# Optimization experiments

Measured on AMD Instinct MI355X. Metric: run time of the kernel, lower is better.

The kernel has to match this reference:

```python
import jax, jax.numpy as jnp
import numpy as np

EPS = 1e-8

def setup_inputs() -> dict:
    key = jax.random.key(0)
    ks = jax.random.split(key, 8)
    B, D, N, F = 8192, 1024, 2048, 8
    d2 = D // 2
    # integer-valued data (IDF acts on integers)
    x = jnp.round(jax.random.normal(ks[0], (B, D), jnp.float32) * 5.0)
    s1 = 1.0 / np.sqrt(d2)
    s2 = 1.0 / np.sqrt(N)
    return {
        "x": x,
        "W1": jax.random.normal(ks[1], (F, d2, N), jnp.float32) * s1,
        "b1": jax.random.normal(ks[2], (F, N), jnp.float32) * 0.01,
        "W2": jax.random.normal(ks[3], (F, N, N), jnp.float32) * s2,
        "b2": jax.random.normal(ks[4], (F, N), jnp.float32) * 0.01,
        "W3": jax.random.normal(ks[5], (F, N, d2), jnp.float32) * s2,
        "b3": jax.random.normal(ks[6], (F, d2), jnp.float32) * 0.01,
        "mean": jnp.zeros((1, D), jnp.float32),
        "log_scale": jnp.ones((1, D), jnp.float32),
    }

def _st_round(v):
    # straight-through round: forward round, identity gradient
    return v + jax.lax.stop_gradient(jnp.round(v) - v)

def _flow(x, W1, b1, W2, b2, W3, b3):
    d2 = x.shape[1] // 2
    def step(z, p):
        w1, bb1, w2, bb2, w3, bb3 = p
        xa, xb = z[:, :d2], z[:, d2:]
        h = jax.nn.leaky_relu(xa @ w1 + bb1)          # [B, N]
        h = jax.nn.leaky_relu(h @ w2 + bb2)           # [B, N]
        t = h @ w3 + bb3                               # [B, d2]
        yb = xb + _st_round(t)
        z = jnp.concatenate([xa, yb], axis=1)[:, ::-1]  # coupling + flip permute
        return z, None
    z, _ = jax.lax.scan(step, x, (W1, b1, W2, b2, W3, b3))
    return z

def reference(x, W1, b1, W2, b2, W3, b3, mean, log_scale):
    z = _flow(x, W1, b1, W2, b2, W3, b3)
    # discretized logistic log-prior: log(sig((z+.5-m)/s) - sig((z-.5-m)/s))
    scale = jnp.exp(log_scale)
    la = jax.nn.log_sigmoid((z + 0.5 - mean) / scale)
    lb = jax.nn.log_sigmoid((z - 0.5 - mean) / scale)
    log_p = la + jnp.log(1.0 - jnp.exp(lb - la) + EPS)  # log_min_exp
    return -log_p.sum(axis=1).mean()  # reduction='avg'
```

## Files before the change

### kernel.cpp

```cpp
#include <hip/hip_runtime.h>
#include <hip/hip_bf16.h>
#include <cmath>


typedef __bf16 bf16_t;
typedef bf16_t bf16x8 __attribute__((ext_vector_type(8)));
typedef float floatx4 __attribute__((ext_vector_type(4)));

#define BQ 8192
#define DD 1024
#define D2 512
#define NH 2048
#define NF 8

__device__ __forceinline__ void gload_lds16(const void* g, void* l) {
    __builtin_amdgcn_global_load_lds(
        (__attribute__((address_space(1))) void*)g,
        (__attribute__((address_space(3))) void*)l, 16, 0, 0);
}

__global__ __launch_bounds__(256)
void transpose_bf16(const float* __restrict__ W, bf16_t* __restrict__ Wt,
                    int K, int N) {
    __shared__ float tile[32][33];
    size_t fo = (size_t)blockIdx.z * K * N;
    int n0 = blockIdx.x * 32, k0 = blockIdx.y * 32;
    int tx = threadIdx.x & 31, ty = threadIdx.x >> 5;
    for (int i = 0; i < 4; i++)
        tile[ty + i*8][tx] = W[fo + (size_t)(k0 + ty + i*8) * N + n0 + tx];
    __syncthreads();
    for (int i = 0; i < 4; i++)
        Wt[fo + (size_t)(n0 + ty + i*8) * K + k0 + tx] = (bf16_t)tile[tx][ty + i*8];
}

__global__ __launch_bounds__(256)
void copy_x(const float4* __restrict__ x, float4* __restrict__ S) {
    int idx = blockIdx.x * blockDim.x + threadIdx.x;
    S[idx] = x[idx];
}

__global__ __launch_bounds__(256)
void prep_A(const float* __restrict__ S, bf16_t* __restrict__ Ab) {
    int idx = blockIdx.x * blockDim.x + threadIdx.x;
    int m = idx >> 9;
    int j = idx & 511;
    Ab[idx] = (bf16_t)S[(size_t)m * DD + j];
}

template<int MODE, int K, int TM, int TN, int MINW>
__global__ __launch_bounds__(256, MINW)
void gemm_kernel(const bf16_t* __restrict__ A, const bf16_t* __restrict__ Bt,
                 const float* __restrict__ bias,
                 bf16_t* __restrict__ Cout, float* __restrict__ S,
                 bf16_t* __restrict__ Abn,
                 int N, int rflag)
{
    constexpr int IM   = TM / 32;
    constexpr int JN   = TN / 32;
    constexpr int NA   = TM / 64;
    constexpr int NBD  = TN / 64;
    constexpr int NDMA = NA + NBD;
    constexpr int T    = K / 32;
    static_assert((T - 1) % 3 == 0, "pipeline triple-unroll needs (T-1)%3==0");
    static_assert(JN % 4 == 0, "bff processed in groups of 4");

    __shared__ __align__(16) bf16_t As[3][TM * 32];
    __shared__ __align__(16) bf16_t Bs[3][TN * 32];

    const int tid  = threadIdx.x;
    const int lane = tid & 63;
    const int wave = tid >> 6;
    const int wm   = wave >> 1;
    const int wn   = wave & 1;
    const int m0   = blockIdx.y * TM;
    const int n0   = blockIdx.x * TN;

    const int srow = tid >> 2;
    const int sq   = ((tid & 3) ^ ((srow >> 1) & 3)) * 8;
    const bf16_t* agp = A  + (size_t)(m0 + srow) * K + sq;
    const bf16_t* bgp = Bt + (size_t)(n0 + srow) * K + sq;

    floatx4 acc[IM][JN];
#pragma unroll
    for (int i = 0; i < IM; i++)
#pragma unroll
        for (int j = 0; j < JN; j++)
            acc[i][j] = (floatx4){0.f, 0.f, 0.f, 0.f};

    const int fr  = lane & 15;
    const int fp8 = ((lane >> 4) ^ ((lane >> 1) & 3)) * 8;

#define ISSUE_TILE(NB)                                                       \
    {                                                                        \
        _Pragma("unroll")                                                    \
        for (int u = 0; u < NA; u++)                                         \
            gload_lds16(agp + (size_t)(u*64) * K, &As[NB][u*2048 + tid*8]);  \
        _Pragma("unroll")                                                    \
        for (int u = 0; u < NBD; u++)                                        \
            gload_lds16(bgp + (size_t)(u*64) * K, &Bs[NB][u*2048 + tid*8]);  \
        agp += 32; bgp += 32;                                                \
    }

#define COMPUTE(CB)                                                          \
    {                                                                        \
        bf16x8 af[IM];                                                       \
        _Pragma("unroll")                                                    \
        for (int i = 0; i < IM; i++)                                         \
            af[i] = *(const bf16x8*)&As[CB][(wm*(TM/2) + i*16 + fr)*32 + fp8];\
        _Pragma("unroll")                                                    \
        for (int g2 = 0; g2 < JN/4; g2++) {                                  \
            bf16x8 bff[4];                                                   \
            _Pragma("unroll")                                                \
            for (int j = 0; j < 4; j++)                                      \
                bff[j] = *(const bf16x8*)                                    \
                    &Bs[CB][(wn*(TN/2) + (g2*4+j)*16 + fr)*32 + fp8];        \
            _Pragma("unroll")                                                \
            for (int i = 0; i < IM; i++)                                     \
                _Pragma("unroll")                                            \
                for (int j = 0; j < 4; j++)                                  \
                    acc[i][g2*4+j] = __builtin_amdgcn_mfma_f32_16x16x32_bf16(\
                                    af[i], bff[j], acc[i][g2*4+j], 0, 0, 0); \
        }                                                                    \
    }

#define PIPE_STEP(NB, CB)                                                    \
    {                                                                        \
        ISSUE_TILE(NB);                                                      \
        __builtin_amdgcn_s_waitcnt(0x0F70 | NDMA);     \
        __builtin_amdgcn_s_barrier();                                        \
        COMPUTE(CB);                                                         \
    }

    ISSUE_TILE(0);

#pragma unroll 1
    for (int g = 0; g < (T - 1) / 3; ++g) {
        PIPE_STEP(1, 0);
        PIPE_STEP(2, 1);
        PIPE_STEP(0, 2);
    }
    __builtin_amdgcn_s_waitcnt(0x0F70);
    __builtin_amdgcn_s_barrier();
    COMPUTE(0);

#undef PIPE_STEP
#undef COMPUTE
#undef ISSUE_TILE

    const int ccol  = lane & 15;
    const int crow4 = (lane >> 4) * 4;
#pragma unroll
    for (int j = 0; j < JN; j++) {
        int col = n0 + wn*(TN/2) + j*16 + ccol;
        float bj = bias[col];
        if (MODE == 0) {
#pragma unroll
            for (int i = 0; i < IM; i++) {
#pragma unroll
                for (int r = 0; r < 4; r++) {
                    int row = m0 + wm*(TM/2) + i*16 + crow4 + r;
                    float v = acc[i][j][r] + bj;
                    v = v >= 0.f ? v : 0.01f * v;
                    Cout[(size_t)row * N + col] = (bf16_t)v;
                }
            }
        } else {
            int slot = rflag ? (511 - col) : (512 + col);
            int aj   = 511 - col;
#pragma unroll
            for (int i = 0; i < IM; i++) {
#pragma unroll
                for (int r = 0; r < 4; r++) {
                    int row = m0 + wm*(TM/2) + i*16 + crow4 + r;
                    float t = acc[i][j][r] + bj;
                    float nv = S[(size_t)row * DD + slot] + rintf(t);
                    S[(size_t)row * DD + slot] = nv;
                    Abn[(size_t)row * D2 + aj] = (bf16_t)nv;
                }
            }
        }
    }
}

__global__ __launch_bounds__(256)
void reduce_nll(const float* __restrict__ S, const float* __restrict__ mean,
                const float* __restrict__ log_scale, float* __restrict__ out)
{
    float local = 0.f;
    const int total = BQ * DD;
    for (int idx = blockIdx.x * blockDim.x + threadIdx.x; idx < total;
         idx += gridDim.x * blockDim.x) {
        int j = idx & (DD - 1);
        float z  = S[idx];
        float mu = mean[j];
        float sc = expf(log_scale[j]);
        float ua = (z + 0.5f - mu) / sc;
        float ub = (z - 0.5f - mu) / sc;
        float la = fminf(ua, 0.f) - log1pf(expf(-fabsf(ua)));
        float lb = fminf(ub, 0.f) - log1pf(expf(-fabsf(ub)));
        float lp = la + logf(1.0f - expf(lb - la) + 1e-8f);
        local += lp;
    }
    __shared__ float red[256];
    red[threadIdx.x] = local;
    __syncthreads();
    for (int s = 128; s > 0; s >>= 1) {
        if (threadIdx.x < s) red[threadIdx.x] += red[threadIdx.x + s];
        __syncthreads();
    }
    if (threadIdx.x == 0) atomicAdd(out, -red[0] * (1.0f / (float)BQ));
}

extern "C" void kernel_launch(void* const* d_in, const int* in_sizes, int n_in,
                              void* d_out, int out_size, void* d_ws, size_t ws_size,
                              hipStream_t stream)
{
    const float* x   = (const float*)d_in[0];
    const float* W1  = (const float*)d_in[1];
    const float* b1  = (const float*)d_in[2];
    const float* W2  = (const float*)d_in[3];
    const float* b2  = (const float*)d_in[4];
    const float* W3  = (const float*)d_in[5];
    const float* b3  = (const float*)d_in[6];
    const float* mean = (const float*)d_in[7];
    const float* lsc  = (const float*)d_in[8];

    char* ws = (char*)d_ws;
    bf16_t* Wt1 = (bf16_t*)ws; ws += (size_t)NF * NH * D2 * 2;
    bf16_t* Wt2 = (bf16_t*)ws; ws += (size_t)NF * NH * NH * 2;
    bf16_t* Wt3 = (bf16_t*)ws; ws += (size_t)NF * D2 * NH * 2;
    float*  S   = (float*)ws;  ws += (size_t)BQ * DD * 4;
    bf16_t* Ab  = (bf16_t*)ws; ws += (size_t)BQ * D2 * 2;
    bf16_t* H1  = (bf16_t*)ws; ws += (size_t)BQ * NH * 2;
    bf16_t* H2  = (bf16_t*)ws;

    hipMemsetAsync(d_out, 0, sizeof(float), stream);

    dim3 blk(256);
    transpose_bf16<<<dim3(NH/32, D2/32, NF), blk, 0, stream>>>(W1, Wt1, D2, NH);
    transpose_bf16<<<dim3(NH/32, NH/32, NF), blk, 0, stream>>>(W2, Wt2, NH, NH);
    transpose_bf16<<<dim3(D2/32, NH/32, NF), blk, 0, stream>>>(W3, Wt3, NH, D2);

    copy_x<<<BQ * DD / 4 / 256, blk, 0, stream>>>((const float4*)x, (float4*)S);
    prep_A<<<BQ * D2 / 256, blk, 0, stream>>>(S, Ab);

    for (int f = 0; f < NF; ++f) {
        int r = f & 1;
        gemm_kernel<0, D2, 128, 256, 2><<<dim3(NH/256, BQ/128), blk, 0, stream>>>(
            Ab, Wt1 + (size_t)f * NH * D2, b1 + (size_t)f * NH, H1, nullptr,
            nullptr, NH, 0);
        gemm_kernel<0, NH, 128, 256, 2><<<dim3(NH/256, BQ/128), blk, 0, stream>>>(
            H1, Wt2 + (size_t)f * NH * NH, b2 + (size_t)f * NH, H2, nullptr,
            nullptr, NH, 0);
        gemm_kernel<1, NH, 64, 128, 3><<<dim3(D2/128, BQ/64), blk, 0, stream>>>(
            H2, Wt3 + (size_t)f * D2 * NH, b3 + (size_t)f * D2, nullptr, S,
            Ab, D2, r);
    }

    reduce_nll<<<2048, blk, 0, stream>>>(S, mean, lsc, (float*)d_out);
}
```

Measured before the change: 1.481 ms.

## Add 256x256-tile 8-wave pipelined GEMM for the two hidden-layer matmuls

Adds a new GEMM kernel with 256x256 output tiles, 512 threads (8 waves), double-buffered LDS fed by direct global-to-LDS loads, and a fine-grained interleaving of LDS reads, next-tile loads and MFMA quarters guarded by barriers and priority hints. It replaces the 128x256 kernel for the first two layers of each flow step. The goal is more data reuse per byte loaded and better overlap of memory traffic with matrix-core work on the dominant N×N GEMM. The cost is a larger LDS footprint (128KB per block) and more registers, which limits occupancy, plus waitcnt constants hand-tuned to the exact load counts.

```diff
diff --git a/kernel.cpp b/kernel.cpp
--- a/kernel.cpp
+++ b/kernel.cpp
@@ -182,6 +182,175 @@
     }
 }
 
+template<int K>
+__global__ __launch_bounds__(512, 2)
+void gemm256_kernel(const bf16_t* __restrict__ A, const bf16_t* __restrict__ Bt,
+                    const float* __restrict__ bias, bf16_t* __restrict__ Cout,
+                    int N)
+{
+    constexpr int T = K / 64;
+    static_assert(T >= 4, "pipeline needs >=4 K-tiles");
+
+    __shared__ __align__(16) bf16_t As[2][16384];
+    __shared__ __align__(16) bf16_t Bs[2][16384];
+
+    const int tid  = threadIdx.x;
+    const int lane = tid & 63;
+    const int wave = tid >> 6;
+    const int wm   = wave >> 2;
+    const int wn   = wave & 3;
+    const int m0   = blockIdx.y * 256;
+    const int n0   = blockIdx.x * 256;
+
+    const int srow = tid >> 3;
+    const int sq   = ((tid & 7) ^ (srow & 7)) * 8;
+    const bf16_t* agp = A  + (size_t)(m0 + srow) * K + sq;
+    const bf16_t* bgp = Bt + (size_t)(n0 + srow) * K + sq;
+    const int ldst = tid * 8;
+
+#define STAGE_A(H, TILE, BUF)                                                 \
+    {                                                                         \
+        _Pragma("unroll")                                                     \
+        for (int u = 0; u < 2; ++u)                                           \
+            gload_lds16(agp + (size_t)((H)*128 + u*64) * K + (size_t)(TILE)*64,\
+                        &As[BUF][(H)*8192 + u*4096 + ldst]);                  \
+    }
+#define STAGE_B(H, TILE, BUF)                                                 \
+    {                                                                         \
+        _Pragma("unroll")                                                     \
+        for (int u = 0; u < 2; ++u)                                           \
+            gload_lds16(bgp + (size_t)((H)*128 + u*64) * K + (size_t)(TILE)*64,\
+                        &Bs[BUF][(H)*8192 + u*4096 + ldst]);                  \
+    }
+#define MFMA16(D, Av, Bv) \
+    D = __builtin_amdgcn_mfma_f32_16x16x32_bf16(Av, Bv, D, 0, 0, 0)
+
+    floatx4 acc[8][4];
+#pragma unroll
+    for (int i = 0; i < 8; ++i)
+#pragma unroll
+        for (int j = 0; j < 4; ++j)
+            acc[i][j] = (floatx4){0.f, 0.f, 0.f, 0.f};
+
+    const int fr = lane & 15;
+    const int l7 = lane & 7;
+    const int qh = lane >> 4;
+    const int ra = (wm*128 + fr) * 64;
+    const int rb = (wn*64  + fr) * 64;
+    const int c0 = ((qh    ) ^ l7) * 8;
+    const int c1 = ((qh + 4) ^ l7) * 8;
+
+    STAGE_B(0, 0, 0); STAGE_B(1, 0, 0);
+    STAGE_A(0, 0, 0); STAGE_A(1, 0, 0);
+    STAGE_B(0, 1, 1); STAGE_B(1, 1, 1);
+    __builtin_amdgcn_s_waitcnt(0x0F74);
+    __builtin_amdgcn_s_barrier();
+
+#pragma unroll 1
+    for (int tau = 0; tau < T; ++tau) {
+        const int c = tau & 1;
+        const bf16_t* Ac = As[c];
+        const bf16_t* Bc = Bs[c];
+        bf16x8 af[4][2], b01[2][2], b23[2][2];
+
+#pragma unroll
+        for (int i = 0; i < 4; ++i) {
+            af[i][0] = *(const bf16x8*)&Ac[ra + i*1024 + c0];
+            af[i][1] = *(const bf16x8*)&Ac[ra + i*1024 + c1];
+        }
+#pragma unroll
+        for (int j = 0; j < 2; ++j) {
+            b01[j][0] = *(const bf16x8*)&Bc[rb + j*1024 + c0];
+            b01[j][1] = *(const bf16x8*)&Bc[rb + j*1024 + c1];
+        }
+        if (tau + 1 < T) STAGE_A(0, tau + 1, c ^ 1);
+        __builtin_amdgcn_s_barrier();
+        __builtin_amdgcn_s_setprio(1);
+#pragma unroll
+        for (int i = 0; i < 4; ++i)
+#pragma unroll
+            for (int j = 0; j < 2; ++j) {
+                MFMA16(acc[i][j], af[i][0], b01[j][0]);
+                MFMA16(acc[i][j], af[i][1], b01[j][1]);
+            }
+        __builtin_amdgcn_s_setprio(0);
+        __builtin_amdgcn_s_barrier();
+
+#pragma unroll
+        for (int j = 0; j < 2; ++j) {
+            b23[j][0] = *(const bf16x8*)&Bc[rb + (j+2)*1024 + c0];
+            b23[j][1] = *(const bf16x8*)&Bc[rb + (j+2)*1024 + c1];
+        }
+        if (tau + 1 < T) STAGE_A(1, tau + 1, c ^ 1);
+        __builtin_amdgcn_s_barrier();
+        __builtin_amdgcn_s_setprio(1);
+#pragma unroll
+        for (int i = 0; i < 4; ++i)
+#pragma unroll
+            for (int j = 0; j < 2; ++j) {
+                MFMA16(acc[i][j+2], af[i][0], b23[j][0]);
+                MFMA16(acc[i][j+2], af[i][1], b23[j][1]);
+            }
+        __builtin_amdgcn_s_setprio(0);
+        __builtin_amdgcn_s_barrier();
+
+#pragma unroll
+        for (int i = 0; i < 4; ++i) {
+            af[i][0] = *(const bf16x8*)&Ac[ra + (i+4)*1024 + c0];
+            af[i][1] = *(const bf16x8*)&Ac[ra + (i+4)*1024 + c1];
+        }
+        if (tau + 2 < T) STAGE_B(0, tau + 2, c);
+        __builtin_amdgcn_s_barrier();
+        __builtin_amdgcn_s_setprio(1);
+#pragma unroll
+        for (int i = 0; i < 4; ++i)
+#pragma unroll
+            for (int j = 0; j < 2; ++j) {
+                MFMA16(acc[i+4][j+2], af[i][0], b23[j][0]);
+                MFMA16(acc[i+4][j+2], af[i][1], b23[j][1]);
+            }
+        __builtin_amdgcn_s_setprio(0);
+        __builtin_amdgcn_s_barrier();
+
+        if (tau + 2 < T) STAGE_B(1, tau + 2, c);
+        __builtin_amdgcn_s_barrier();
+        __builtin_amdgcn_s_setprio(1);
+#pragma unroll
+        for (int i = 0; i < 4; ++i)
+#pragma unroll
+            for (int j = 0; j < 2; ++j) {
+                MFMA16(acc[i+4][j], af[i][0], b01[j][0]);
+                MFMA16(acc[i+4][j], af[i][1], b01[j][1]);
+            }
+        __builtin_amdgcn_s_setprio(0);
+        if (tau < T - 2)       __builtin_amdgcn_s_waitcnt(0x0F74);
+        else if (tau == T - 2) __builtin_amdgcn_s_waitcnt(0x0F70);
+        __builtin_amdgcn_s_barrier();
+    }
+
+#undef STAGE_A
+#undef STAGE_B
+#undef MFMA16
+
+    const int ccol  = lane & 15;
+    const int crow4 = (lane >> 4) * 4;
+#pragma unroll
+    for (int j = 0; j < 4; ++j) {
+        int col = n0 + wn*64 + j*16 + ccol;
+        float bj = bias[col];
+#pragma unroll
+        for (int i = 0; i < 8; ++i) {
+#pragma unroll
+            for (int r = 0; r < 4; ++r) {
+                int row = m0 + wm*128 + i*16 + crow4 + r;
+                float v = acc[i][j][r] + bj;
+                v = v >= 0.f ? v : 0.01f * v;
+                Cout[(size_t)row * N + col] = (bf16_t)v;
+            }
+        }
+    }
+}
+
 __global__ __launch_bounds__(256)
 void reduce_nll(const float* __restrict__ S, const float* __restrict__ mean,
                 const float* __restrict__ log_scale, float* __restrict__ out)
@@ -246,12 +415,10 @@
 
     for (int f = 0; f < NF; ++f) {
         int r = f & 1;
-        gemm_kernel<0, D2, 128, 256, 2><<<dim3(NH/256, BQ/128), blk, 0, stream>>>(
-            Ab, Wt1 + (size_t)f * NH * D2, b1 + (size_t)f * NH, H1, nullptr,
-            nullptr, NH, 0);
-        gemm_kernel<0, NH, 128, 256, 2><<<dim3(NH/256, BQ/128), blk, 0, stream>>>(
-            H1, Wt2 + (size_t)f * NH * NH, b2 + (size_t)f * NH, H2, nullptr,
-            nullptr, NH, 0);
+        gemm256_kernel<D2><<<dim3(NH/256, BQ/256), dim3(512), 0, stream>>>(
+            Ab, Wt1 + (size_t)f * NH * D2, b1 + (size_t)f * NH, H1, NH);
+        gemm256_kernel<NH><<<dim3(NH/256, BQ/256), dim3(512), 0, stream>>>(
+            H1, Wt2 + (size_t)f * NH * NH, b2 + (size_t)f * NH, H2, NH);
         gemm_kernel<1, NH, 64, 128, 3><<<dim3(D2/128, BQ/64), blk, 0, stream>>>(
             H2, Wt3 + (size_t)f * D2 * NH, b3 + (size_t)f * D2, nullptr, S,
             Ab, D2, r);
```

Result: slower. 1.602 ms (+8.2%).

## Add double-buffered 128x128 GEMM for hidden layers and fuse input prep kernels

Applied to the files above, without the earlier changes.

Adds a new GEMM kernel with a simple two-stage LDS double buffer (async global-to-LDS loads of the next K tile overlapped with MFMA compute on the current one). The first two hidden-layer GEMMs use it with 128x128 tiles in place of the 128x256 triple-stage pipelined kernel, which doubles the grid size. The copy_x and prep_A kernels are also merged into one init kernel that writes both the float state and the bf16 half. Smaller tiles raise occupancy and parallelism but reduce reuse of each loaded tile, and the shallower pipeline may hide less memory latency.

```diff
diff --git a/kernel.cpp b/kernel.cpp
--- a/kernel.cpp
+++ b/kernel.cpp
@@ -4,6 +4,7 @@
 
 
 typedef __bf16 bf16_t;
+typedef bf16_t bf16x4 __attribute__((ext_vector_type(4)));
 typedef bf16_t bf16x8 __attribute__((ext_vector_type(8)));
 typedef float floatx4 __attribute__((ext_vector_type(4)));
 
@@ -34,17 +35,19 @@
 }
 
 __global__ __launch_bounds__(256)
-void copy_x(const float4* __restrict__ x, float4* __restrict__ S) {
+void init_SA(const float4* __restrict__ x, float4* __restrict__ S,
+             bf16_t* __restrict__ Ab) {
     int idx = blockIdx.x * blockDim.x + threadIdx.x;
-    S[idx] = x[idx];
-}
-
-__global__ __launch_bounds__(256)
-void prep_A(const float* __restrict__ S, bf16_t* __restrict__ Ab) {
-    int idx = blockIdx.x * blockDim.x + threadIdx.x;
-    int m = idx >> 9;
-    int j = idx & 511;
-    Ab[idx] = (bf16_t)S[(size_t)m * DD + j];
+    float4 v = x[idx];
+    S[idx] = v;
+    int col4 = idx & (DD/4 - 1);
+    if (col4 < D2/4) {
+        int m = idx >> 8;
+        bf16x4 p;
+        p[0] = (bf16_t)v.x; p[1] = (bf16_t)v.y;
+        p[2] = (bf16_t)v.z; p[3] = (bf16_t)v.w;
+        ((bf16x4*)Ab)[(size_t)m * (D2/4) + col4] = p;
+    }
 }
 
 template<int MODE, int K, int TM, int TN, int MINW>
@@ -177,6 +180,115 @@
                     S[(size_t)row * DD + slot] = nv;
                     Abn[(size_t)row * D2 + aj] = (bf16_t)nv;
                 }
+            }
+        }
+    }
+}
+
+template<int K, int TM, int TN>
+__global__ __launch_bounds__(256, 2)
+void gemm2b_kernel(const bf16_t* __restrict__ A, const bf16_t* __restrict__ Bt,
+                   const float* __restrict__ bias, bf16_t* __restrict__ Cout,
+                   int N)
+{
+    constexpr int IM   = TM / 32;
+    constexpr int JN   = TN / 32;
+    constexpr int NA   = TM / 64;
+    constexpr int NBD  = TN / 64;
+    constexpr int T    = K / 32;
+    static_assert(T >= 2, "need >=2 K-tiles");
+    static_assert(JN % 4 == 0, "bff processed in groups of 4");
+
+    __shared__ __align__(16) bf16_t As[2][TM * 32];
+    __shared__ __align__(16) bf16_t Bs[2][TN * 32];
+
+    const int tid  = threadIdx.x;
+    const int lane = tid & 63;
+    const int wave = tid >> 6;
+    const int wm   = wave >> 1;
+    const int wn   = wave & 1;
+    const int m0   = blockIdx.y * TM;
+    const int n0   = blockIdx.x * TN;
+
+    const int srow = tid >> 2;
+    const int sq   = ((tid & 3) ^ ((srow >> 1) & 3)) * 8;
+    const bf16_t* agp = A  + (size_t)(m0 + srow) * K + sq;
+    const bf16_t* bgp = Bt + (size_t)(n0 + srow) * K + sq;
+
+    floatx4 acc[IM][JN];
+#pragma unroll
+    for (int i = 0; i < IM; i++)
+#pragma unroll
+        for (int j = 0; j < JN; j++)
+            acc[i][j] = (floatx4){0.f, 0.f, 0.f, 0.f};
+
+    const int fr  = lane & 15;
+    const int fp8 = ((lane >> 4) ^ ((lane >> 1) & 3)) * 8;
+
+#define ISSUE_TILE(NB)                                                       \
+    {                                                                        \
+        _Pragma("unroll")                                                    \
+        for (int u = 0; u < NA; u++)                                         \
+            gload_lds16(agp + (size_t)(u*64) * K, &As[NB][u*2048 + tid*8]);  \
+        _Pragma("unroll")                                                    \
+        for (int u = 0; u < NBD; u++)                                        \
+            gload_lds16(bgp + (size_t)(u*64) * K, &Bs[NB][u*2048 + tid*8]);  \
+        agp += 32; bgp += 32;                                                \
+    }
+
+#define COMPUTE(CB)                                                          \
+    {                                                                        \
+        bf16x8 af[IM];                                                       \
+        _Pragma("unroll")                                                    \
+        for (int i = 0; i < IM; i++)                                         \
+            af[i] = *(const bf16x8*)&As[CB][(wm*(TM/2) + i*16 + fr)*32 + fp8];\
+        _Pragma("unroll")                                                    \
+        for (int g2 = 0; g2 < JN/4; g2++) {                                  \
+            bf16x8 bff[4];                                                   \
+            _Pragma("unroll")                                                \
+            for (int j = 0; j < 4; j++)                                      \
+                bff[j] = *(const bf16x8*)                                    \
+                    &Bs[CB][(wn*(TN/2) + (g2*4+j)*16 + fr)*32 + fp8];        \
+            _Pragma("unroll")                                                \
+            for (int i = 0; i < IM; i++)                                     \
+                _Pragma("unroll")                                            \
+                for (int j = 0; j < 4; j++)                                  \
+                    acc[i][g2*4+j] = __builtin_amdgcn_mfma_f32_16x16x32_bf16(\
+                                    af[i], bff[j], acc[i][g2*4+j], 0, 0, 0); \
+        }                                                                    \
+    }
+
+    ISSUE_TILE(0);
+    __builtin_amdgcn_s_waitcnt(0x0F70);
+    __builtin_amdgcn_s_barrier();
+
+#pragma unroll 1
+    for (int tau = 0; tau < T; ++tau) {
+        if (tau + 1 < T) ISSUE_TILE((tau + 1) & 1);
+        COMPUTE(tau & 1);
+        if (tau + 1 < T) {
+            __builtin_amdgcn_s_waitcnt(0x0F70);
+            __builtin_amdgcn_s_barrier();
+        }
+    }
+
+#undef COMPUTE
+#undef ISSUE_TILE
+
+    const int ccol  = lane & 15;
+    const int crow4 = (lane >> 4) * 4;
+#pragma unroll
+    for (int j = 0; j < JN; j++) {
+        int col = n0 + wn*(TN/2) + j*16 + ccol;
+        float bj = bias[col];
+#pragma unroll
+        for (int i = 0; i < IM; i++) {
+#pragma unroll
+            for (int r = 0; r < 4; r++) {
+                int row = m0 + wm*(TM/2) + i*16 + crow4 + r;
+                float v = acc[i][j][r] + bj;
+                v = v >= 0.f ? v : 0.01f * v;
+                Cout[(size_t)row * N + col] = (bf16_t)v;
             }
         }
     }
@@ -241,17 +353,14 @@
     transpose_bf16<<<dim3(NH/32, NH/32, NF), blk, 0, stream>>>(W2, Wt2, NH, NH);
     transpose_bf16<<<dim3(D2/32, NH/32, NF), blk, 0, stream>>>(W3, Wt3, NH, D2);
 
-    copy_x<<<BQ * DD / 4 / 256, blk, 0, stream>>>((const float4*)x, (float4*)S);
-    prep_A<<<BQ * D2 / 256, blk, 0, stream>>>(S, Ab);
+    init_SA<<<BQ * DD / 4 / 256, blk, 0, stream>>>((const float4*)x, (float4*)S, Ab);
 
     for (int f = 0; f < NF; ++f) {
         int r = f & 1;
-        gemm_kernel<0, D2, 128, 256, 2><<<dim3(NH/256, BQ/128), blk, 0, stream>>>(
-            Ab, Wt1 + (size_t)f * NH * D2, b1 + (size_t)f * NH, H1, nullptr,
-            nullptr, NH, 0);
-        gemm_kernel<0, NH, 128, 256, 2><<<dim3(NH/256, BQ/128), blk, 0, stream>>>(
-            H1, Wt2 + (size_t)f * NH * NH, b2 + (size_t)f * NH, H2, nullptr,
-            nullptr, NH, 0);
+        gemm2b_kernel<D2, 128, 128><<<dim3(NH/128, BQ/128), blk, 0, stream>>>(
+            Ab, Wt1 + (size_t)f * NH * D2, b1 + (size_t)f * NH, H1, NH);
+        gemm2b_kernel<NH, 128, 128><<<dim3(NH/128, BQ/128), blk, 0, stream>>>(
+            H1, Wt2 + (size_t)f * NH * NH, b2 + (size_t)f * NH, H2, NH);
         gemm_kernel<1, NH, 64, 128, 3><<<dim3(D2/128, BQ/64), blk, 0, stream>>>(
             H2, Wt3 + (size_t)f * D2 * NH, b3 + (size_t)f * D2, nullptr, S,
             Ab, D2, r);
```

After: 1.587 ms. 1.07x slower.

## Split-K the third GEMM with separate epilogue kernel and fuse input prep

Applied to the files above, without the earlier changes.

The third GEMM of each flow step (K=2048, N=512) switches from 64x128 tiles to 128x128 tiles split into two K halves along grid z. Each half writes fp32 partial sums into a buffer that reuses the H1 workspace, and a new epilogue kernel adds the partials and bias, rounds, and updates S and the bf16 A buffer. The aim is to recover parallelism and tile efficiency on the narrow GEMM, at the cost of an extra launch and extra fp32 traffic per step. The copy_x and prep_A kernels are also fused into one init kernel.

```diff
diff --git a/kernel.cpp b/kernel.cpp
--- a/kernel.cpp
+++ b/kernel.cpp
@@ -4,6 +4,7 @@
 
 
 typedef __bf16 bf16_t;
+typedef bf16_t bf16x4 __attribute__((ext_vector_type(4)));
 typedef bf16_t bf16x8 __attribute__((ext_vector_type(8)));
 typedef float floatx4 __attribute__((ext_vector_type(4)));
 
@@ -34,34 +35,36 @@
 }
 
 __global__ __launch_bounds__(256)
-void copy_x(const float4* __restrict__ x, float4* __restrict__ S) {
+void init_SA(const float4* __restrict__ x, float4* __restrict__ S,
+             bf16_t* __restrict__ Ab) {
     int idx = blockIdx.x * blockDim.x + threadIdx.x;
-    S[idx] = x[idx];
-}
-
-__global__ __launch_bounds__(256)
-void prep_A(const float* __restrict__ S, bf16_t* __restrict__ Ab) {
-    int idx = blockIdx.x * blockDim.x + threadIdx.x;
-    int m = idx >> 9;
-    int j = idx & 511;
-    Ab[idx] = (bf16_t)S[(size_t)m * DD + j];
-}
-
-template<int MODE, int K, int TM, int TN, int MINW>
+    float4 v = x[idx];
+    S[idx] = v;
+    int col4 = idx & (DD/4 - 1);
+    if (col4 < D2/4) {
+        int m = idx >> 8;
+        bf16x4 p;
+        p[0] = (bf16_t)v.x; p[1] = (bf16_t)v.y;
+        p[2] = (bf16_t)v.z; p[3] = (bf16_t)v.w;
+        ((bf16x4*)Ab)[(size_t)m * (D2/4) + col4] = p;
+    }
+}
+
+template<int MODE, int KSTR, int KDEP, int TM, int TN, int MINW>
 __global__ __launch_bounds__(256, MINW)
 void gemm_kernel(const bf16_t* __restrict__ A, const bf16_t* __restrict__ Bt,
                  const float* __restrict__ bias,
-                 bf16_t* __restrict__ Cout, float* __restrict__ S,
-                 bf16_t* __restrict__ Abn,
-                 int N, int rflag)
+                 bf16_t* __restrict__ Cout, float* __restrict__ Pout,
+                 int N)
 {
     constexpr int IM   = TM / 32;
     constexpr int JN   = TN / 32;
     constexpr int NA   = TM / 64;
     constexpr int NBD  = TN / 64;
     constexpr int NDMA = NA + NBD;
-    constexpr int T    = K / 32;
-    static_assert((T - 1) % 3 == 0, "pipeline triple-unroll needs (T-1)%3==0");
+    constexpr int T    = KDEP / 32;
+    constexpr int REM  = (T - 1) % 3;
+    static_assert(REM == 0 || REM == 1, "tail handles rem 0/1 only");
     static_assert(JN % 4 == 0, "bff processed in groups of 4");
 
     __shared__ __align__(16) bf16_t As[3][TM * 32];
@@ -74,11 +77,12 @@
     const int wn   = wave & 1;
     const int m0   = blockIdx.y * TM;
     const int n0   = blockIdx.x * TN;
+    const int koff = (MODE == 2) ? blockIdx.z * KDEP : 0;
 
     const int srow = tid >> 2;
     const int sq   = ((tid & 3) ^ ((srow >> 1) & 3)) * 8;
-    const bf16_t* agp = A  + (size_t)(m0 + srow) * K + sq;
-    const bf16_t* bgp = Bt + (size_t)(n0 + srow) * K + sq;
+    const bf16_t* agp = A  + (size_t)(m0 + srow) * KSTR + koff + sq;
+    const bf16_t* bgp = Bt + (size_t)(n0 + srow) * KSTR + koff + sq;
 
     floatx4 acc[IM][JN];
 #pragma unroll
@@ -94,10 +98,10 @@
     {                                                                        \
         _Pragma("unroll")                                                    \
         for (int u = 0; u < NA; u++)                                         \
-            gload_lds16(agp + (size_t)(u*64) * K, &As[NB][u*2048 + tid*8]);  \
+            gload_lds16(agp + (size_t)(u*64) * KSTR, &As[NB][u*2048 + tid*8]);\
         _Pragma("unroll")                                                    \
         for (int u = 0; u < NBD; u++)                                        \
-            gload_lds16(bgp + (size_t)(u*64) * K, &Bs[NB][u*2048 + tid*8]);  \
+            gload_lds16(bgp + (size_t)(u*64) * KSTR, &Bs[NB][u*2048 + tid*8]);\
         agp += 32; bgp += 32;                                                \
     }
 
@@ -139,9 +143,10 @@
         PIPE_STEP(2, 1);
         PIPE_STEP(0, 2);
     }
+    if constexpr (REM == 1) { PIPE_STEP(1, 0); }
     __builtin_amdgcn_s_waitcnt(0x0F70);
     __builtin_amdgcn_s_barrier();
-    COMPUTE(0);
+    COMPUTE(REM == 1 ? 1 : 0);
 
 #undef PIPE_STEP
 #undef COMPUTE
@@ -152,8 +157,8 @@
 #pragma unroll
     for (int j = 0; j < JN; j++) {
         int col = n0 + wn*(TN/2) + j*16 + ccol;
-        float bj = bias[col];
         if (MODE == 0) {
+            float bj = bias[col];
 #pragma unroll
             for (int i = 0; i < IM; i++) {
 #pragma unroll
@@ -165,20 +170,41 @@
                 }
             }
         } else {
-            int slot = rflag ? (511 - col) : (512 + col);
-            int aj   = 511 - col;
+            float* P = Pout + (size_t)blockIdx.z * BQ * N;
 #pragma unroll
             for (int i = 0; i < IM; i++) {
 #pragma unroll
                 for (int r = 0; r < 4; r++) {
                     int row = m0 + wm*(TM/2) + i*16 + crow4 + r;
-                    float t = acc[i][j][r] + bj;
-                    float nv = S[(size_t)row * DD + slot] + rintf(t);
-                    S[(size_t)row * DD + slot] = nv;
-                    Abn[(size_t)row * D2 + aj] = (bf16_t)nv;
+                    P[(size_t)row * N + col] = acc[i][j][r];
                 }
             }
         }
+    }
+}
+
+__global__ __launch_bounds__(256)
+void g3_epilogue(const float* __restrict__ P, const float* __restrict__ b3,
+                 float* __restrict__ S, bf16_t* __restrict__ Ab, int rflag)
+{
+    int idx = blockIdx.x * blockDim.x + threadIdx.x;
+    int row = idx >> 7;
+    int c4  = (idx & 127) * 4;
+    float4 p0 = ((const float4*)P)[idx];
+    float4 p1 = ((const float4*)(P + (size_t)BQ * D2))[idx];
+    float4 bb = ((const float4*)b3)[idx & 127];
+    float t0 = p0.x + p1.x + bb.x;
+    float t1 = p0.y + p1.y + bb.y;
+    float t2 = p0.z + p1.z + bb.z;
+    float t3 = p0.w + p1.w + bb.w;
+    const float tv[4] = {t0, t1, t2, t3};
+#pragma unroll
+    for (int e = 0; e < 4; ++e) {
+        int col  = c4 + e;
+        int slot = rflag ? (511 - col) : (512 + col);
+        float nv = S[(size_t)row * DD + slot] + rintf(tv[e]);
+        S[(size_t)row * DD + slot] = nv;
+        Ab[(size_t)row * D2 + (511 - col)] = (bf16_t)nv;
     }
 }
 
@@ -233,6 +259,7 @@
     bf16_t* Ab  = (bf16_t*)ws; ws += (size_t)BQ * D2 * 2;
     bf16_t* H1  = (bf16_t*)ws; ws += (size_t)BQ * NH * 2;
     bf16_t* H2  = (bf16_t*)ws;
+    float*  P3  = (float*)H1;
 
     hipMemsetAsync(d_out, 0, sizeof(float), stream);
 
@@ -241,20 +268,18 @@
     transpose_bf16<<<dim3(NH/32, NH/32, NF), blk, 0, stream>>>(W2, Wt2, NH, NH);
     transpose_bf16<<<dim3(D2/32, NH/32, NF), blk, 0, stream>>>(W3, Wt3, NH, D2);
 
-    copy_x<<<BQ * DD / 4 / 256, blk, 0, stream>>>((const float4*)x, (float4*)S);
-    prep_A<<<BQ * D2 / 256, blk, 0, stream>>>(S, Ab);
+    init_SA<<<BQ * DD / 4 / 256, blk, 0, stream>>>((const float4*)x, (float4*)S, Ab);
 
     for (int f = 0; f < NF; ++f) {
         int r = f & 1;
-        gemm_kernel<0, D2, 128, 256, 2><<<dim3(NH/256, BQ/128), blk, 0, stream>>>(
-            Ab, Wt1 + (size_t)f * NH * D2, b1 + (size_t)f * NH, H1, nullptr,
-            nullptr, NH, 0);
-        gemm_kernel<0, NH, 128, 256, 2><<<dim3(NH/256, BQ/128), blk, 0, stream>>>(
-            H1, Wt2 + (size_t)f * NH * NH, b2 + (size_t)f * NH, H2, nullptr,
-            nullptr, NH, 0);
-        gemm_kernel<1, NH, 64, 128, 3><<<dim3(D2/128, BQ/64), blk, 0, stream>>>(
-            H2, Wt3 + (size_t)f * D2 * NH, b3 + (size_t)f * D2, nullptr, S,
-            Ab, D2, r);
+        gemm_kernel<0, D2, D2, 128, 256, 2><<<dim3(NH/256, BQ/128), blk, 0, stream>>>(
+            Ab, Wt1 + (size_t)f * NH * D2, b1 + (size_t)f * NH, H1, nullptr, NH);
+        gemm_kernel<0, NH, NH, 128, 256, 2><<<dim3(NH/256, BQ/128), blk, 0, stream>>>(
+            H1, Wt2 + (size_t)f * NH * NH, b2 + (size_t)f * NH, H2, nullptr, NH);
+        gemm_kernel<2, NH, 1024, 128, 128, 2><<<dim3(D2/128, BQ/128, 2), blk, 0, stream>>>(
+            H2, Wt3 + (size_t)f * D2 * NH, nullptr, nullptr, P3, D2);
+        g3_epilogue<<<BQ * D2 / 4 / 256, blk, 0, stream>>>(
+            P3, b3 + (size_t)f * D2, S, Ab, r);
     }
 
     reduce_nll<<<2048, blk, 0, stream>>>(S, mean, lsc, (float*)d_out);
```

Measured after the change: 1.510 ms. About the same (+1.9%).
